# Optimization experiments

Hardware: AMD Instinct MI355X
Metric: run time of the kernel (lower is better)

## Reference

```python
import jax, jax.numpy as jnp
import numpy as np

N_HEADS = 32
HEAD_DIM = 64
D_STATE = 128
D_CONV = 4
CHUNK = 64
EPS = 1e-6


def _dwconv(u, k, b):
    # depthwise 1D conv, SAME padding; u: (B,L,C), k: (K,1,C)
    y = jax.lax.conv_general_dilated(
        u, k, (1,), 'SAME',
        dimension_numbers=('NWC', 'WIO', 'NWC'),
        feature_group_count=u.shape[-1])
    return y + b


def _segsum(a):
    # a: (..., T) -> (..., T, T) with seg[i,j] = sum_{k=j+1..i} a[k], -inf above diag
    T = a.shape[-1]
    ac = jnp.cumsum(a, axis=-1)
    seg = ac[..., :, None] - ac[..., None, :]
    mask = jnp.tril(jnp.ones((T, T), dtype=bool))
    return jnp.where(mask, seg, -jnp.inf)


def _ssd(x, A, Bm, Cm, chunk):
    # x: (b,l,h,p), A: (b,l,h), Bm/Cm: (b,l,n) (head dim of 1 squeezed)
    b, l, h, p = x.shape
    c = l // chunk
    xch = x.reshape(b, c, chunk, h, p)
    Ach = A.reshape(b, c, chunk, h).transpose(0, 3, 1, 2)  # (b,h,c,l)
    Bch = Bm.reshape(b, c, chunk, -1)
    Cch = Cm.reshape(b, c, chunk, -1)
    A_cs = jnp.cumsum(Ach, axis=-1)  # (b,h,c,l)
    # 1. intra-chunk (diagonal blocks)
    Lmat = jnp.exp(_segsum(Ach))  # (b,h,c,l,s)
    Y_diag = jnp.einsum('bcln,bcsn,bhcls,bcshp->bclhp', Cch, Bch, Lmat, xch)
    # 2. states at chunk boundaries
    decay_states = jnp.exp(A_cs[..., -1:] - A_cs)  # (b,h,c,l)
    states = jnp.einsum('bcln,bhcl,bclhp->bchpn', Bch, decay_states, xch)
    # 3. inter-chunk recurrence
    A_last = jnp.pad(A_cs[..., -1], ((0, 0), (0, 0), (1, 0)))  # (b,h,c+1)
    decay_chunk = jnp.exp(_segsum(A_last))  # (b,h,c+1,c+1)
    states0 = jnp.concatenate([jnp.zeros_like(states[:, :1]), states], axis=1)
    new_states = jnp.einsum('bhzc,bchpn->bzhpn', decay_chunk, states0)
    prev_states, final_state = new_states[:, :-1], new_states[:, -1]
    # 4. state -> output
    state_decay = jnp.exp(A_cs)  # (b,h,c,l)
    Y_off = jnp.einsum('bcln,bchpn,bhcl->bclhp', Cch, prev_states, state_decay)
    Y = (Y_diag + Y_off).reshape(b, l, h, p)
    return Y, final_state


def setup_inputs() -> dict:
    key = jax.random.key(0)
    ks = jax.random.split(key, 10)
    B, L, D_MODEL, D_INNER = 4, 4096, 1024, 2048
    x = jax.random.normal(ks[0], (B, L, D_MODEL), jnp.float32)
    W_in = jax.random.normal(ks[1], (D_MODEL, 2 * D_INNER), jnp.float32) * 0.02
    conv_x_k = jax.random.normal(ks[2], (D_CONV, 1, D_INNER), jnp.float32) * 0.2
    conv_x_b = jnp.zeros((D_INNER,), jnp.float32)
    conv_z_k = jax.random.normal(ks[3], (D_CONV, 1, D_INNER), jnp.float32) * 0.2
    conv_z_b = jnp.zeros((D_INNER,), jnp.float32)
    W_x = jax.random.normal(ks[4], (D_INNER, N_HEADS + 2 * D_STATE), jnp.float32) * 0.02
    dt = jnp.exp(jax.random.uniform(ks[5], (N_HEADS,)) * (np.log(0.1) - np.log(0.001)) + np.log(0.001))
    dt = jnp.clip(dt, 1e-4)
    dt_bias = dt + jnp.log(-jnp.expm1(-dt))
    A_log = jnp.log(jax.random.uniform(ks[6], (N_HEADS,), minval=1.0, maxval=16.0))
    D = jnp.ones((N_HEADS,), jnp.float32)
    norm_w = jnp.ones((D_INNER,), jnp.float32)
    W_out = jax.random.normal(ks[7], (D_INNER, D_MODEL), jnp.float32) * 0.02
    return {"x": x, "W_in": W_in, "conv_x_k": conv_x_k, "conv_x_b": conv_x_b,
            "conv_z_k": conv_z_k, "conv_z_b": conv_z_b, "W_x": W_x,
            "dt_bias": dt_bias, "A_log": A_log, "D": D, "norm_w": norm_w,
            "W_out": W_out}


def reference(x, W_in, conv_x_k, conv_x_b, conv_z_k, conv_z_b, W_x,
              dt_bias, A_log, D, norm_w, W_out):
    b, L, _ = x.shape
    A = -jnp.exp(A_log)  # (h,)
    xz = x @ W_in
    u, z = jnp.split(xz, 2, axis=-1)
    u = jax.nn.silu(_dwconv(u, conv_x_k, conv_x_b))
    z = jax.nn.silu(_dwconv(z, conv_z_k, conv_z_b))
    x_dbl = u @ W_x  # (b,l,h+2n)
    dt = jax.nn.softplus(x_dbl[..., :N_HEADS] + dt_bias)  # (b,l,h)
    Bm = x_dbl[..., N_HEADS:N_HEADS + D_STATE]
    Cm = x_dbl[..., N_HEADS + D_STATE:]
    uh = u.reshape(b, L, N_HEADS, HEAD_DIM)
    y, _ = _ssd(uh * dt[..., None], A * dt, Bm, Cm, CHUNK)
    y = y + uh * D[..., None]
    y = y.reshape(b, L, -1)
    # gated RMSNorm: gate then normalize
    y = y * jax.nn.silu(z)
    y = y * jax.lax.rsqrt(jnp.mean(y * y, axis=-1, keepdims=True) + EPS) * norm_w
    return y @ W_out
```

## Files before the change

### kernel.cpp

```cpp
#include <hip/hip_runtime.h>
#include <hip/hip_bf16.h>

#define BATCH   4
#define SEQL    4096
#define DMODEL  1024
#define DINNER  2048
#define NHEADS  32
#define HEADD   64
#define DSTATE  128
#define NCHUNK  64
#define CHUNK   64
#define BL      (BATCH * SEQL)
#define XDBLW   (NHEADS + 2 * DSTATE)
#define GC      32
#define NGROUP  2

typedef __hip_bfloat16 bf16;
typedef __attribute__((ext_vector_type(8))) short s16x8;
typedef __attribute__((ext_vector_type(8))) unsigned short u16x8;
typedef __attribute__((ext_vector_type(4))) float f32x4;

__device__ __forceinline__ float silu_f(float x) {
    return x / (1.f + expf(-x));
}
__device__ __forceinline__ float toF(float x) { return x; }
__device__ __forceinline__ float toF(bf16 x)  { return __bfloat162float(x); }
__device__ __forceinline__ void stF(float* p, float v) { *p = v; }
__device__ __forceinline__ void stF(bf16* p, float v)  { *p = __float2bfloat16(v); }
__device__ __forceinline__ float bfbits2f(unsigned short b) {
    unsigned int u = ((unsigned int)b) << 16;
    return __builtin_bit_cast(float, u);
}

__global__ __launch_bounds__(256) void f32_to_bf16_kernel(
    const float* __restrict__ in, bf16* __restrict__ out, size_t n)
{
    const size_t i = ((size_t)blockIdx.x * 256 + threadIdx.x) * 4;
    if (i >= n) return;
    const float4 v = *(const float4*)(in + i);
    bf16 o[4];
    o[0] = __float2bfloat16(v.x); o[1] = __float2bfloat16(v.y);
    o[2] = __float2bfloat16(v.z); o[3] = __float2bfloat16(v.w);
    __builtin_memcpy(&out[i], o, 8);
}

__global__ __launch_bounds__(256) void transpose_to_bf16_kernel(
    const float* __restrict__ in, bf16* __restrict__ out,
    int R, int C, int Cpad)
{
    __shared__ float t[32][33];
    const int c0 = blockIdx.x * 32, r0 = blockIdx.y * 32;
    const int tx = threadIdx.x & 31, ty = threadIdx.x >> 5;
    #pragma unroll
    for (int i = 0; i < 4; i++) {
        const int r = r0 + ty + i * 8, c = c0 + tx;
        t[ty + i * 8][tx] = (c < C) ? in[(size_t)r * C + c] : 0.f;
    }
    __syncthreads();
    #pragma unroll
    for (int i = 0; i < 4; i++) {
        const int c = c0 + ty + i * 8, r = r0 + tx;
        out[(size_t)c * R + r] = __float2bfloat16(t[tx][ty + i * 8]);
    }
}

template <typename TC>
__global__ __launch_bounds__(256) void mfma_gemm(
    const bf16* __restrict__ A, const bf16* __restrict__ Bt,
    TC* __restrict__ C, int M, int Nout, int K, int lda, int ldb, int ldc)
{
    __shared__ __align__(16) bf16 As[4096];
    __shared__ __align__(16) bf16 Bs[4096];
    const int tid = threadIdx.x;
    const int m0 = blockIdx.y * 128;
    const int n0 = blockIdx.x * 128;
    const int wave = tid >> 6, lane = tid & 63;
    const int wr = wave >> 1, wc = wave & 1;
    const int fr = lane & 15;
    const int fq = lane >> 4;

    f32x4 acc[4][4];
    #pragma unroll
    for (int i = 0; i < 4; i++)
        #pragma unroll
        for (int j = 0; j < 4; j++)
            acc[i][j] = (f32x4){0.f, 0.f, 0.f, 0.f};

    const int srow = tid & 127;
    const int sk0 = (tid >> 7) * 8;
    const bf16* Ag = A + (size_t)(m0 + srow) * lda + sk0;
    const bf16* Bg = Bt + (size_t)(n0 + srow) * ldb + sk0;
    const int lb = (wave >> 1) * 1024 + (wave & 1) * 512;

    for (int k0 = 0; k0 < K; k0 += 32) {
        __syncthreads();
        #pragma unroll
        for (int i = 0; i < 2; i++) {
            __builtin_amdgcn_global_load_lds(
                (const __attribute__((address_space(1))) unsigned int*)(Ag + k0 + i * 16),
                (__attribute__((address_space(3))) unsigned int*)(As + i * 2048 + lb),
                16, 0, 0);
            __builtin_amdgcn_global_load_lds(
                (const __attribute__((address_space(1))) unsigned int*)(Bg + k0 + i * 16),
                (__attribute__((address_space(3))) unsigned int*)(Bs + i * 2048 + lb),
                16, 0, 0);
        }
        __syncthreads();

        s16x8 af[4], bfv[4];
        #pragma unroll
        for (int mi = 0; mi < 4; mi++)
            af[mi] = *(const s16x8*)&As[fq * 1024 + (wr * 64 + mi * 16 + fr) * 8];
        #pragma unroll
        for (int ni = 0; ni < 4; ni++)
            bfv[ni] = *(const s16x8*)&Bs[fq * 1024 + (wc * 64 + ni * 16 + fr) * 8];
        #pragma unroll
        for (int mi = 0; mi < 4; mi++)
            #pragma unroll
            for (int ni = 0; ni < 4; ni++)
                acc[mi][ni] = __builtin_amdgcn_mfma_f32_16x16x32_bf16(
                    af[mi], bfv[ni], acc[mi][ni], 0, 0, 0);
    }

    #pragma unroll
    for (int mi = 0; mi < 4; mi++) {
        #pragma unroll
        for (int ni = 0; ni < 4; ni++) {
            const int col = n0 + wc * 64 + ni * 16 + fr;
            if (col < Nout) {
                #pragma unroll
                for (int r = 0; r < 4; r++) {
                    const int row = m0 + wr * 64 + mi * 16 + fq * 4 + r;
                    stF(&C[(size_t)row * ldc + col], acc[mi][ni][r]);
                }
            }
        }
    }
}

__global__ __launch_bounds__(256) void conv_one_kernel(
    const bf16* __restrict__ in,
    const float* __restrict__ kern, const float* __restrict__ bias,
    bf16* __restrict__ out)
{
    const size_t gid = (size_t)blockIdx.x * 256 + threadIdx.x;
    const int d0 = ((int)(gid & 255)) << 3;
    const size_t row = gid >> 8;
    const int l = (int)(row & (SEQL - 1));
    const size_t bL = row - l;
    float a[8];
    #pragma unroll
    for (int j = 0; j < 8; j++) a[j] = bias[d0 + j];
    #pragma unroll
    for (int w = 0; w < 4; w++) {
        const int ls = l + w - 1;
        if (ls >= 0 && ls < SEQL) {
            u16x8 v;
            __builtin_memcpy(&v, &in[(bL + ls) * DINNER + d0], 16);
            #pragma unroll
            for (int j = 0; j < 8; j++)
                a[j] = fmaf(bfbits2f(v[j]), kern[w * DINNER + d0 + j], a[j]);
        }
    }
    bf16 ov[8];
    #pragma unroll
    for (int j = 0; j < 8; j++) ov[j] = __float2bfloat16(silu_f(a[j]));
    __builtin_memcpy(&out[row * DINNER + d0], ov, 16);
}

__global__ __launch_bounds__(256) void dt_kernel(
    const float* __restrict__ x_dbl,
    const float* __restrict__ dt_bias, const float* __restrict__ A_log,
    float* __restrict__ dtb, float* __restrict__ dacs, float* __restrict__ ctot)
{
    const int bid = blockIdx.x;
    const int hg = bid & 7;
    const int bc = bid >> 3;
    const int c = bc & (NCHUNK - 1);
    const int b = bc >> 6;
    const int w = threadIdx.x >> 6, lane = threadIdx.x & 63;
    const int h = hg * 4 + w;
    const size_t row = (size_t)b * SEQL + c * CHUNK + lane;

    const float raw = x_dbl[row * XDBLW + h] + dt_bias[h];
    const float dt = (raw > 20.f) ? raw : log1pf(expf(raw));
    dtb[row * NHEADS + h] = dt;

    float s = -expf(A_log[h]) * dt;
    #pragma unroll
    for (int off = 1; off < 64; off <<= 1) {
        const float t = __shfl_up(s, off);
        if (lane >= off) s += t;
    }
    dacs[row * NHEADS + h] = s;
    if (lane == 63) ctot[((size_t)b * NHEADS + h) * NCHUNK + c] = s;
}

__global__ __launch_bounds__(256) void ssd_states_kernel(
    const bf16* __restrict__ u, const float* __restrict__ x_dbl,
    const float* __restrict__ dtb, const float* __restrict__ dacs,
    bf16* __restrict__ stG, int g)
{
    __shared__ float Bd[64][132];
    __shared__ float xs[64][68];
    __shared__ float csL[64], dtL[64], eD[64];
    const int h = blockIdx.x, cg = blockIdx.y, b = blockIdx.z;
    const int c = g * GC + cg;
    const int tid = threadIdx.x;
    const size_t row0 = (size_t)b * SEQL + c * CHUNK;

    if (tid < 64) {
        csL[tid] = dacs[(row0 + tid) * NHEADS + h];
        dtL[tid] = dtb[(row0 + tid) * NHEADS + h];
    }
    __syncthreads();
    if (tid < 64) eD[tid] = expf(csL[63] - csL[tid]) * dtL[tid];
    __syncthreads();

    #pragma unroll
    for (int j = 0; j < 8; j++) {
        const int f = j * 256 + tid;
        const int l = f >> 5, n0 = (f & 31) * 4;
        const float4 v = *(const float4*)&x_dbl[(row0 + l) * XDBLW + NHEADS + n0];
        const float e = eD[l];
        Bd[l][n0]     = v.x * e; Bd[l][n0 + 1] = v.y * e;
        Bd[l][n0 + 2] = v.z * e; Bd[l][n0 + 3] = v.w * e;
    }
    #pragma unroll
    for (int j = 0; j < 2; j++) {
        const int f = j * 256 + tid;
        const int l = f >> 3, p0 = (f & 7) * 8;
        u16x8 v;
        __builtin_memcpy(&v, &u[(row0 + l) * DINNER + h * HEADD + p0], 16);
        #pragma unroll
        for (int i = 0; i < 8; i++) xs[l][p0 + i] = bfbits2f(v[i]);
    }
    __syncthreads();

    const int pq = tid >> 5, ng = tid & 31;
    float acc[8][4] = {};
    #pragma unroll 8
    for (int l = 0; l < 64; l++) {
        const float4 bv = *(const float4*)&Bd[l][ng * 4];
        const float4 x0 = *(const float4*)&xs[l][pq * 8];
        const float4 x1 = *(const float4*)&xs[l][pq * 8 + 4];
        const float xv[8] = {x0.x, x0.y, x0.z, x0.w, x1.x, x1.y, x1.z, x1.w};
        const float bb[4] = {bv.x, bv.y, bv.z, bv.w};
        #pragma unroll
        for (int pp = 0; pp < 8; pp++)
            #pragma unroll
            for (int nn = 0; nn < 4; nn++)
                acc[pp][nn] = fmaf(xv[pp], bb[nn], acc[pp][nn]);
    }

    const size_t base = (((size_t)b * NHEADS + h) * GC + cg) * 8192;
    #pragma unroll
    for (int pp = 0; pp < 8; pp++) {
        bf16 ov[4];
        #pragma unroll
        for (int nn = 0; nn < 4; nn++) ov[nn] = __float2bfloat16(acc[pp][nn]);
        __builtin_memcpy(&stG[base + (pq * 8 + pp) * 128 + ng * 4], ov, 8);
    }
}

__global__ __launch_bounds__(256) void ssd_scan_kernel(
    bf16* __restrict__ stG, const float* __restrict__ ctot,
    float* __restrict__ runbuf, int g)
{
    const int q = blockIdx.x & 3, bh = blockIdx.x >> 2;
    const int b = bh >> 5, h = bh & 31;
    const int off = q * 2048 + threadIdx.x * 8;
    float run[8];
    if (g == 0) {
        #pragma unroll
        for (int i = 0; i < 8; i++) run[i] = 0.f;
    } else {
        const float4 r0 = *(const float4*)&runbuf[(size_t)bh * 8192 + off];
        const float4 r1 = *(const float4*)&runbuf[(size_t)bh * 8192 + off + 4];
        run[0]=r0.x; run[1]=r0.y; run[2]=r0.z; run[3]=r0.w;
        run[4]=r1.x; run[5]=r1.y; run[6]=r1.z; run[7]=r1.w;
    }
    const float* ct = ctot + ((size_t)b * NHEADS + h) * NCHUNK + g * GC;
    const size_t base = (size_t)bh * GC * 8192 + off;
    for (int c = 0; c < GC; c++) {
        u16x8 sv;
        __builtin_memcpy(&sv, &stG[base + (size_t)c * 8192], 16);
        bf16 pv[8];
        #pragma unroll
        for (int i = 0; i < 8; i++) pv[i] = __float2bfloat16(run[i]);
        __builtin_memcpy(&stG[base + (size_t)c * 8192], pv, 16);
        const float dc = expf(ct[c]);
        #pragma unroll
        for (int i = 0; i < 8; i++)
            run[i] = fmaf(run[i], dc, bfbits2f(sv[i]));
    }
    *(float4*)&runbuf[(size_t)bh * 8192 + off]     = make_float4(run[0], run[1], run[2], run[3]);
    *(float4*)&runbuf[(size_t)bh * 8192 + off + 4] = make_float4(run[4], run[5], run[6], run[7]);
}

__global__ __launch_bounds__(256) void ssd_fused_kernel(
    const bf16* __restrict__ u, const float* __restrict__ x_dbl,
    const float* __restrict__ dtb, const float* __restrict__ dacs,
    const float* __restrict__ Dv, const bf16* __restrict__ stG,
    bf16* __restrict__ y, int g)
{
    __shared__ __align__(16) bf16 Cs[64 * 152];
    __shared__ __align__(16) bf16 Bp[64 * 152];
    __shared__ __align__(16) bf16 xT[64 * 88];
    __shared__ __align__(16) bf16 Ms[64 * 88];
    __shared__ float csA[64], dtl[64], eC[64];

    const int h = blockIdx.x, cg = blockIdx.y, b = blockIdx.z;
    const int c = g * GC + cg;
    const int tid = threadIdx.x;
    const int wl = tid >> 6, lane = tid & 63;
    const int fr = lane & 15, fq = lane >> 4;
    const size_t row0 = (size_t)b * SEQL + c * CHUNK;

    if (tid < 64) {
        csA[tid] = dacs[(row0 + tid) * NHEADS + h];
        dtl[tid] = dtb[(row0 + tid) * NHEADS + h];
    }
    #pragma unroll
    for (int j = 0; j < 8; j++) {
        const int f = j * 256 + tid;
        const int l = f >> 5, n0 = (f & 31) * 4;
        const float4 cv = *(const float4*)&x_dbl[(row0 + l) * XDBLW + NHEADS + DSTATE + n0];
        const float4 bv = *(const float4*)&x_dbl[(row0 + l) * XDBLW + NHEADS + n0];
        bf16 ct[4] = {__float2bfloat16(cv.x), __float2bfloat16(cv.y),
                      __float2bfloat16(cv.z), __float2bfloat16(cv.w)};
        bf16 bt[4] = {__float2bfloat16(bv.x), __float2bfloat16(bv.y),
                      __float2bfloat16(bv.z), __float2bfloat16(bv.w)};
        __builtin_memcpy(&Cs[l * 152 + n0], ct, 8);
        __builtin_memcpy(&Bp[l * 152 + n0], bt, 8);
    }
    #pragma unroll
    for (int j = 0; j < 2; j++) {
        const int f = j * 256 + tid;
        const int l = f >> 3, p0 = (f & 7) * 8;
        u16x8 v;
        __builtin_memcpy(&v, &u[(row0 + l) * DINNER + h * HEADD + p0], 16);
        #pragma unroll
        for (int i = 0; i < 8; i++)
            xT[(p0 + i) * 88 + l] = __builtin_bit_cast(bf16, (unsigned short)v[i]);
    }
    __syncthreads();
    if (tid < 64) eC[tid] = expf(csA[tid]);

    f32x4 sf[4];
    #pragma unroll
    for (int ni = 0; ni < 4; ni++) sf[ni] = (f32x4){0.f, 0.f, 0.f, 0.f};
    #pragma unroll
    for (int kk = 0; kk < 4; kk++) {
        const s16x8 af = *(const s16x8*)&Cs[(wl * 16 + fr) * 152 + kk * 32 + fq * 8];
        #pragma unroll
        for (int ni = 0; ni < 4; ni++) {
            const s16x8 bv = *(const s16x8*)&Bp[(ni * 16 + fr) * 152 + kk * 32 + fq * 8];
            sf[ni] = __builtin_amdgcn_mfma_f32_16x16x32_bf16(af, bv, sf[ni], 0, 0, 0);
        }
    }
    #pragma unroll
    for (int ni = 0; ni < 4; ni++) {
        const int s = ni * 16 + fr;
        #pragma unroll
        for (int r = 0; r < 4; r++) {
            const int l = wl * 16 + fq * 4 + r;
            float v = 0.f;
            if (l >= s) v = sf[ni][r] * expf(csA[l] - csA[s]) * dtl[s];
            Ms[l * 88 + s] = __float2bfloat16(v);
        }
    }
    __syncthreads();
    const size_t sbase = (((size_t)b * NHEADS + h) * GC + cg) * 8192;
    #pragma unroll
    for (int j = 0; j < 4; j++) {
        const int f = j * 256 + tid;
        const int p = f >> 4, n0 = (f & 15) * 8;
        u16x8 v;
        __builtin_memcpy(&v, &stG[sbase + p * 128 + n0], 16);
        __builtin_memcpy(&Bp[p * 152 + n0], &v, 16);
    }
    __syncthreads();

    f32x4 ady[4], aof[4];
    #pragma unroll
    for (int ni = 0; ni < 4; ni++) {
        ady[ni] = (f32x4){0.f, 0.f, 0.f, 0.f};
        aof[ni] = (f32x4){0.f, 0.f, 0.f, 0.f};
    }
    #pragma unroll
    for (int kk = 0; kk < 2; kk++) {
        const s16x8 af = *(const s16x8*)&Ms[(wl * 16 + fr) * 88 + kk * 32 + fq * 8];
        #pragma unroll
        for (int ni = 0; ni < 4; ni++) {
            const s16x8 bv = *(const s16x8*)&xT[(ni * 16 + fr) * 88 + kk * 32 + fq * 8];
            ady[ni] = __builtin_amdgcn_mfma_f32_16x16x32_bf16(af, bv, ady[ni], 0, 0, 0);
        }
    }
    #pragma unroll
    for (int kk = 0; kk < 4; kk++) {
        const s16x8 af = *(const s16x8*)&Cs[(wl * 16 + fr) * 152 + kk * 32 + fq * 8];
        #pragma unroll
        for (int ni = 0; ni < 4; ni++) {
            const s16x8 bv = *(const s16x8*)&Bp[(ni * 16 + fr) * 152 + kk * 32 + fq * 8];
            aof[ni] = __builtin_amdgcn_mfma_f32_16x16x32_bf16(af, bv, aof[ni], 0, 0, 0);
        }
    }
    const float Dh = Dv[h];
    #pragma unroll
    for (int ni = 0; ni < 4; ni++) {
        const int p = ni * 16 + fr;
        #pragma unroll
        for (int r = 0; r < 4; r++) {
            const int l = wl * 16 + fq * 4 + r;
            const float uval = toF(xT[p * 88 + l]);
            const float val = ady[ni][r] + eC[l] * aof[ni][r] + Dh * uval;
            y[(row0 + l) * DINNER + h * HEADD + p] = __float2bfloat16(val);
        }
    }
}

__global__ __launch_bounds__(256) void gate_norm_kernel(
    bf16* __restrict__ y, const bf16* __restrict__ z,
    const float* __restrict__ norm_w)
{
    __shared__ float red[4];
    const size_t row = blockIdx.x;
    const int tid = threadIdx.x;
    const int d0 = tid * 8;
    u16x8 yv, zv;
    __builtin_memcpy(&yv, &y[row * DINNER + d0], 16);
    __builtin_memcpy(&zv, &z[row * DINNER + d0], 16);
    float v[8];
    float ss = 0.f;
    #pragma unroll
    for (int j = 0; j < 8; j++) {
        const float val = bfbits2f(yv[j]) * silu_f(bfbits2f(zv[j]));
        v[j] = val;
        ss = fmaf(val, val, ss);
    }
    #pragma unroll
    for (int off = 32; off > 0; off >>= 1) ss += __shfl_down(ss, off);
    const int lane = tid & 63, w = tid >> 6;
    if (lane == 0) red[w] = ss;
    __syncthreads();
    const float tot = red[0] + red[1] + red[2] + red[3];
    const float scale = rsqrtf(tot / (float)DINNER + 1e-6f);
    bf16 ov[8];
    #pragma unroll
    for (int j = 0; j < 8; j++)
        ov[j] = __float2bfloat16(v[j] * scale * norm_w[d0 + j]);
    __builtin_memcpy(&y[row * DINNER + d0], ov, 16);
}

extern "C" void kernel_launch(void* const* d_in, const int* in_sizes, int n_in,
                              void* d_out, int out_size, void* d_ws, size_t ws_size,
                              hipStream_t stream)
{
    const float* x       = (const float*)d_in[0];
    const float* W_in    = (const float*)d_in[1];
    const float* conv_xk = (const float*)d_in[2];
    const float* conv_xb = (const float*)d_in[3];
    const float* conv_zk = (const float*)d_in[4];
    const float* conv_zb = (const float*)d_in[5];
    const float* W_x     = (const float*)d_in[6];
    const float* dt_bias = (const float*)d_in[7];
    const float* A_log   = (const float*)d_in[8];
    const float* Dv      = (const float*)d_in[9];
    const float* norm_w  = (const float*)d_in[10];
    const float* W_out   = (const float*)d_in[11];
    float* out = (float*)d_out;
    char* ws   = (char*)d_ws;

    if (ws_size < (size_t)234389504) return;
    bf16*  xbf    = (bf16*)(ws);
    bf16*  W_inT  = (bf16*)(ws + 33554432);
    bf16*  u      = (bf16*)(ws);
    bf16*  z      = (bf16*)(ws + 67108864);
    bf16*  scr    = (bf16*)(ws + 134217728);
    float* x_dbl  = (float*)(ws + 201326592);
    float* dtb    = (float*)(ws + 220200960);
    float* dacs   = (float*)(ws + 222298112);
    float* ctot   = (float*)(ws + 224395264);
    bf16*  W_xT   = (bf16*)(ws + 224428032);
    bf16*  W_outT = (bf16*)(ws + 226000896);
    float* runbuf = (float*)(ws + 230195200);
    bf16* stG = scr;
    bf16* y   = u;

    f32_to_bf16_kernel<<<16384, 256, 0, stream>>>(x, xbf, (size_t)BL * DMODEL);
    transpose_to_bf16_kernel<<<dim3(128, 32), 256, 0, stream>>>(
        W_in, W_inT, DMODEL, 2 * DINNER, 2 * DINNER);
    transpose_to_bf16_kernel<<<dim3(12, 64), 256, 0, stream>>>(
        W_x, W_xT, DINNER, XDBLW, 384);
    transpose_to_bf16_kernel<<<dim3(32, 64), 256, 0, stream>>>(
        W_out, W_outT, DINNER, DMODEL, DMODEL);

    mfma_gemm<bf16><<<dim3(16, 128), 256, 0, stream>>>(
        xbf, W_inT + (size_t)DINNER * DMODEL, scr, BL, DINNER, DMODEL,
        DMODEL, DMODEL, DINNER);
    conv_one_kernel<<<BL, 256, 0, stream>>>(scr, conv_zk, conv_zb, z);
    mfma_gemm<bf16><<<dim3(16, 128), 256, 0, stream>>>(
        xbf, W_inT, scr, BL, DINNER, DMODEL, DMODEL, DMODEL, DINNER);
    conv_one_kernel<<<BL, 256, 0, stream>>>(scr, conv_xk, conv_xb, u);
    mfma_gemm<float><<<dim3(3, 128), 256, 0, stream>>>(
        u, W_xT, x_dbl, BL, XDBLW, DINNER, DINNER, DINNER, XDBLW);
    dt_kernel<<<BATCH * NCHUNK * 8, 256, 0, stream>>>(
        x_dbl, dt_bias, A_log, dtb, dacs, ctot);
    for (int g = 0; g < NGROUP; g++) {
        ssd_states_kernel<<<dim3(NHEADS, GC, BATCH), 256, 0, stream>>>(
            u, x_dbl, dtb, dacs, stG, g);
        ssd_scan_kernel<<<512, 256, 0, stream>>>(stG, ctot, runbuf, g);
        ssd_fused_kernel<<<dim3(NHEADS, GC, BATCH), 256, 0, stream>>>(
            u, x_dbl, dtb, dacs, Dv, stG, y, g);
    }
    gate_norm_kernel<<<BL, 256, 0, stream>>>(y, z, norm_w);
    mfma_gemm<float><<<dim3(8, 128), 256, 0, stream>>>(
        y, W_outT, out, BL, DMODEL, DINNER, DINNER, DINNER, DMODEL);
}
```

Measured before the change: 1.146 ms.

## Use MFMA for SSD chunk-state outer products and swizzle GEMM blocks across XCDs

The chunk-state kernel previously computed x^T·(decayed B) with scalar FP32 FMAs from float shared-memory tiles. It now stores transposed bf16 tiles and uses 16x16x32 bf16 MFMA instructions, so inputs are rounded to bf16 before accumulation. Separately, the GEMM block index is remapped so consecutive tiles land on the same XCD, aiming for better L2 locality. The stores of state results become scalar 2-byte writes, which may be less coalesced than before.

Result: faster. 1.096 ms (-4.4%).

```diff
diff --git a/kernel.cpp b/kernel.cpp
--- a/kernel.cpp
+++ b/kernel.cpp
@@ -72,8 +72,15 @@
     __shared__ __align__(16) bf16 As[4096];
     __shared__ __align__(16) bf16 Bs[4096];
     const int tid = threadIdx.x;
-    const int m0 = blockIdx.y * 128;
-    const int n0 = blockIdx.x * 128;
+
+    const int nwg = gridDim.x * gridDim.y;
+    const int orig = blockIdx.y * gridDim.x + blockIdx.x;
+    const int q = nwg >> 3, r = nwg & 7;
+    const int xcd = orig & 7, loc = orig >> 3;
+    const int swz = (xcd < r ? xcd * (q + 1) : r * (q + 1) + (xcd - r) * q) + loc;
+    const int m0 = (swz / gridDim.x) * 128;
+    const int n0 = (swz % gridDim.x) * 128;
+
     const int wave = tid >> 6, lane = tid & 63;
     const int wr = wave >> 1, wc = wave & 1;
     const int fr = lane & 15;
@@ -129,9 +136,9 @@
             const int col = n0 + wc * 64 + ni * 16 + fr;
             if (col < Nout) {
                 #pragma unroll
-                for (int r = 0; r < 4; r++) {
-                    const int row = m0 + wr * 64 + mi * 16 + fq * 4 + r;
-                    stF(&C[(size_t)row * ldc + col], acc[mi][ni][r]);
+                for (int r2 = 0; r2 < 4; r2++) {
+                    const int row = m0 + wr * 64 + mi * 16 + fq * 4 + r2;
+                    stF(&C[(size_t)row * ldc + col], acc[mi][ni][r2]);
                 }
             }
         }
@@ -201,12 +208,14 @@
     const float* __restrict__ dtb, const float* __restrict__ dacs,
     bf16* __restrict__ stG, int g)
 {
-    __shared__ float Bd[64][132];
-    __shared__ float xs[64][68];
+    __shared__ __align__(16) bf16 Bdt[128 * 72];
+    __shared__ __align__(16) bf16 xT[64 * 72];
     __shared__ float csL[64], dtL[64], eD[64];
     const int h = blockIdx.x, cg = blockIdx.y, b = blockIdx.z;
     const int c = g * GC + cg;
     const int tid = threadIdx.x;
+    const int wv = tid >> 6, lane = tid & 63;
+    const int fr = lane & 15, fq = lane >> 4;
     const size_t row0 = (size_t)b * SEQL + c * CHUNK;
 
     if (tid < 64) {
@@ -223,8 +232,10 @@
         const int l = f >> 5, n0 = (f & 31) * 4;
         const float4 v = *(const float4*)&x_dbl[(row0 + l) * XDBLW + NHEADS + n0];
         const float e = eD[l];
-        Bd[l][n0]     = v.x * e; Bd[l][n0 + 1] = v.y * e;
-        Bd[l][n0 + 2] = v.z * e; Bd[l][n0 + 3] = v.w * e;
+        Bdt[(n0    ) * 72 + l] = __float2bfloat16(v.x * e);
+        Bdt[(n0 + 1) * 72 + l] = __float2bfloat16(v.y * e);
+        Bdt[(n0 + 2) * 72 + l] = __float2bfloat16(v.z * e);
+        Bdt[(n0 + 3) * 72 + l] = __float2bfloat16(v.w * e);
     }
     #pragma unroll
     for (int j = 0; j < 2; j++) {
@@ -233,34 +244,41 @@
         u16x8 v;
         __builtin_memcpy(&v, &u[(row0 + l) * DINNER + h * HEADD + p0], 16);
         #pragma unroll
-        for (int i = 0; i < 8; i++) xs[l][p0 + i] = bfbits2f(v[i]);
-    }
-    __syncthreads();
-
-    const int pq = tid >> 5, ng = tid & 31;
-    float acc[8][4] = {};
-    #pragma unroll 8
-    for (int l = 0; l < 64; l++) {
-        const float4 bv = *(const float4*)&Bd[l][ng * 4];
-        const float4 x0 = *(const float4*)&xs[l][pq * 8];
-        const float4 x1 = *(const float4*)&xs[l][pq * 8 + 4];
-        const float xv[8] = {x0.x, x0.y, x0.z, x0.w, x1.x, x1.y, x1.z, x1.w};
-        const float bb[4] = {bv.x, bv.y, bv.z, bv.w};
-        #pragma unroll
-        for (int pp = 0; pp < 8; pp++)
+        for (int i = 0; i < 8; i++)
+            xT[(p0 + i) * 72 + l] = __builtin_bit_cast(bf16, (unsigned short)v[i]);
+    }
+    __syncthreads();
+
+    f32x4 acc[4][2];
+    #pragma unroll
+    for (int mi = 0; mi < 4; mi++)
+        #pragma unroll
+        for (int ni = 0; ni < 2; ni++)
+            acc[mi][ni] = (f32x4){0.f, 0.f, 0.f, 0.f};
+    #pragma unroll
+    for (int kk = 0; kk < 2; kk++) {
+        s16x8 bv0 = *(const s16x8*)&Bdt[(wv * 32 + fr) * 72 + kk * 32 + fq * 8];
+        s16x8 bv1 = *(const s16x8*)&Bdt[(wv * 32 + 16 + fr) * 72 + kk * 32 + fq * 8];
+        #pragma unroll
+        for (int mi = 0; mi < 4; mi++) {
+            const s16x8 af = *(const s16x8*)&xT[(mi * 16 + fr) * 72 + kk * 32 + fq * 8];
+            acc[mi][0] = __builtin_amdgcn_mfma_f32_16x16x32_bf16(af, bv0, acc[mi][0], 0, 0, 0);
+            acc[mi][1] = __builtin_amdgcn_mfma_f32_16x16x32_bf16(af, bv1, acc[mi][1], 0, 0, 0);
+        }
+    }
+
+    const size_t base = (((size_t)b * NHEADS + h) * GC + cg) * 8192;
+    #pragma unroll
+    for (int mi = 0; mi < 4; mi++)
+        #pragma unroll
+        for (int ni = 0; ni < 2; ni++) {
+            const int n = wv * 32 + ni * 16 + fr;
             #pragma unroll
-            for (int nn = 0; nn < 4; nn++)
-                acc[pp][nn] = fmaf(xv[pp], bb[nn], acc[pp][nn]);
-    }
-
-    const size_t base = (((size_t)b * NHEADS + h) * GC + cg) * 8192;
-    #pragma unroll
-    for (int pp = 0; pp < 8; pp++) {
-        bf16 ov[4];
-        #pragma unroll
-        for (int nn = 0; nn < 4; nn++) ov[nn] = __float2bfloat16(acc[pp][nn]);
-        __builtin_memcpy(&stG[base + (pq * 8 + pp) * 128 + ng * 4], ov, 8);
-    }
+            for (int r = 0; r < 4; r++) {
+                const int p = mi * 16 + fq * 4 + r;
+                stG[base + p * 128 + n] = __float2bfloat16(acc[mi][ni][r]);
+            }
+        }
 }
 
 __global__ __launch_bounds__(256) void ssd_scan_kernel(
```
